# Kernel tuning notes

Hardware: AMD Instinct MI355X
Metric: run time of the kernel (lower is better)

The kernel has to match this reference:

```python
import jax, jax.numpy as jnp
import numpy as np

B, S, DIM, N_CONCEPTS, N_LAYERS = 4, 2048, 1024, 2048, 2


def _phase_linear(x, W, b):
    # x: [b,s,d_in,2]; same real linear applied to real and imag components
    return jnp.einsum('bsdp,od->bsop', x, W) + b[:, None]


def _phase_layernorm(x, gamma, beta, eps=1e-5):
    # per-component LayerNorm over the feature dim with shared affine params
    mu = x.mean(axis=-2, keepdims=True)
    var = x.var(axis=-2, keepdims=True)
    return (x - mu) / jnp.sqrt(var + eps) * gamma[:, None] + beta[:, None]


def setup_inputs() -> dict:
    key = jax.random.key(0)
    ks = jax.random.split(key, 8)
    x = jax.random.normal(ks[0], (B, S, DIM, 2), dtype=jnp.float32)
    concept_memory = jax.random.normal(ks[1], (N_CONCEPTS, DIM, 2), dtype=jnp.float32) * 0.02
    scale = 1.0 / np.sqrt(DIM)
    W_layers = jax.random.normal(ks[2], (N_LAYERS, DIM, DIM), dtype=jnp.float32) * scale
    b_layers = jnp.zeros((N_LAYERS, DIM), dtype=jnp.float32)
    gamma = jnp.ones((N_LAYERS, DIM), dtype=jnp.float32)
    beta = jnp.zeros((N_LAYERS, DIM), dtype=jnp.float32)
    W_out = jax.random.normal(ks[3], (DIM, DIM), dtype=jnp.float32) * scale
    b_out = jnp.zeros((DIM,), dtype=jnp.float32)
    g_out = jnp.ones((DIM,), dtype=jnp.float32)
    beta_out = jnp.zeros((DIM,), dtype=jnp.float32)
    return {"x": x, "concept_memory": concept_memory, "W_layers": W_layers,
            "b_layers": b_layers, "gamma": gamma, "beta": beta,
            "W_out": W_out, "b_out": b_out, "g_out": g_out, "beta_out": beta_out}


def reference(x, concept_memory, W_layers, b_layers, gamma, beta, W_out, b_out, g_out, beta_out):
    xr, xi = x[..., 0], x[..., 1]                       # [b,s,d]
    cr, ci = concept_memory[..., 0], concept_memory[..., 1]  # [n,d]
    # phase-coherence concept attention
    dot_real = jnp.einsum('bsd,nd->bsn', xr, cr) + jnp.einsum('bsd,nd->bsn', xi, ci)
    x_mag = jnp.sqrt((xr ** 2 + xi ** 2).sum(axis=-1, keepdims=True) + 1e-8)   # [b,s,1]
    c_mag = jnp.sqrt((cr ** 2 + ci ** 2).sum(axis=-1) + 1e-8)                  # [n]
    coherence = dot_real / (x_mag * c_mag[None, None, :] + 1e-8)
    concept_attn = jax.nn.softmax(coherence * 2.0, axis=-1)
    concept_retrieved = jnp.einsum('bsn,ndp->bsdp', concept_attn, concept_memory)
    h = x + concept_retrieved * 0.1
    # gated FFN blocks (eval mode: dropout off)
    for l in range(N_LAYERS):
        residual = h
        h = _phase_layernorm(h, gamma[l], beta[l])
        h = _phase_linear(h, W_layers[l], b_layers[l])
        h = jax.nn.gelu(h[..., 0:1], approximate=False) * h
        h = residual + h * 0.1
    out = _phase_layernorm(h, g_out, beta_out)
    out = _phase_linear(out, W_out, b_out)
    return out
```

## Files before the change

### kernel.cpp

```cpp
#include <hip/hip_runtime.h>
#include <hip/hip_bf16.h>

#define ROWS 8192
#define K2   2048
#define NCPT 2048
#define DIMD 1024

using short8 = __attribute__((ext_vector_type(8))) short;
using f32x4  = __attribute__((ext_vector_type(4))) float;

__device__ __forceinline__ unsigned short f2b(float f) {
  __hip_bfloat16 h = __float2bfloat16(f);
  return *reinterpret_cast<unsigned short*>(&h);
}
__device__ __forceinline__ float b2f(unsigned short u) {
  unsigned int x = ((unsigned int)u) << 16;
  return __uint_as_float(x);
}

__device__ __forceinline__ void store_bf16x8(unsigned short* dst, const float4& a, const float4& b) {
  union { unsigned short u[8]; uint4 q; } p;
  p.u[0]=f2b(a.x); p.u[1]=f2b(a.y); p.u[2]=f2b(a.z); p.u[3]=f2b(a.w);
  p.u[4]=f2b(b.x); p.u[5]=f2b(b.y); p.u[6]=f2b(b.z); p.u[7]=f2b(b.w);
  *reinterpret_cast<uint4*>(dst) = p.q;
}
__device__ __forceinline__ void store_bf16x4(unsigned short* dst, float a, float b, float c, float d) {
  union { unsigned short u[4]; uint2 q; } p;
  p.u[0]=f2b(a); p.u[1]=f2b(b); p.u[2]=f2b(c); p.u[3]=f2b(d);
  *reinterpret_cast<uint2*>(dst) = p.q;
}

__device__ __forceinline__ void async_lds16(const void* g, void* l) {
  __builtin_amdgcn_global_load_lds((__attribute__((address_space(1))) void*)g,
                                   (__attribute__((address_space(3))) void*)l, 16, 0, 0);
}

__global__ void cast_row_mag(const float* __restrict__ src, unsigned short* __restrict__ dst,
                             float* __restrict__ mag, int ncol) {
  __shared__ float sred[4];
  int row = blockIdx.x, t = threadIdx.x;
  const float* s = src + (size_t)row * ncol;
  unsigned short* d = dst + (size_t)row * ncol;
  float ss = 0.f;
  for (int i = t * 8; i < ncol; i += 2048) {
    float4 a = *(const float4*)(s + i);
    float4 b = *(const float4*)(s + i + 4);
    ss += a.x*a.x + a.y*a.y + a.z*a.z + a.w*a.w;
    ss += b.x*b.x + b.y*b.y + b.z*b.z + b.w*b.w;
    store_bf16x8(d + i, a, b);
  }
  int lane = t & 63, w = t >> 6;
  for (int o = 32; o; o >>= 1) ss += __shfl_down(ss, o);
  if (lane == 0) sred[w] = ss;
  __syncthreads();
  if (t == 0) mag[row] = sqrtf(sred[0] + sred[1] + sred[2] + sred[3] + 1e-8f);
}

__global__ void cast_f2b(const float* __restrict__ src, unsigned short* __restrict__ dst, int n) {
  int stride = gridDim.x * blockDim.x * 8;
  for (int i = (blockIdx.x * blockDim.x + threadIdx.x) * 8; i < n; i += stride) {
    float4 a = *(const float4*)(src + i);
    float4 b = *(const float4*)(src + i + 4);
    store_bf16x8(dst + i, a, b);
  }
}

__global__ void transpose_f2b(const float* __restrict__ src, unsigned short* __restrict__ dst, int n) {
  __shared__ float tile[32][33];
  int bx = blockIdx.x * 32;
  int by = blockIdx.y * 32;
  int tx = threadIdx.x & 31, ty = threadIdx.x >> 5;
  #pragma unroll
  for (int i = ty; i < 32; i += 8)
    tile[i][tx] = src[(size_t)(by + i) * n + bx + tx];
  __syncthreads();
  #pragma unroll
  for (int i = ty; i < 32; i += 8)
    dst[(size_t)(bx + i) * n + by + tx] = f2b(tile[tx][i]);
}

__global__ void softmax_attn(const unsigned short* __restrict__ logit, unsigned short* __restrict__ attn) {
  __shared__ float sred[4];
  int row = blockIdx.x, t = threadIdx.x;
  int lane = t & 63, w = t >> 6;
  const unsigned short* lr = logit + (size_t)row * NCPT + t * 8;
  short8 lv = *reinterpret_cast<const short8*>(lr);
  float l[8];
  #pragma unroll
  for (int i = 0; i < 8; ++i) l[i] = b2f((unsigned short)lv[i]);
  float m = l[0];
  #pragma unroll
  for (int i = 1; i < 8; ++i) m = fmaxf(m, l[i]);
  for (int o = 32; o; o >>= 1) m = fmaxf(m, __shfl_down(m, o));
  if (lane == 0) sred[w] = m;
  __syncthreads();
  m = fmaxf(fmaxf(sred[0], sred[1]), fmaxf(sred[2], sred[3]));
  __syncthreads();
  float e[8], s = 0.f;
  #pragma unroll
  for (int i = 0; i < 8; ++i) { e[i] = expf(l[i] - m); s += e[i]; }
  for (int o = 32; o; o >>= 1) s += __shfl_down(s, o);
  if (lane == 0) sred[w] = s;
  __syncthreads();
  s = sred[0] + sred[1] + sred[2] + sred[3];
  float inv = 1.f / s;
  float4 A = make_float4(e[0]*inv, e[1]*inv, e[2]*inv, e[3]*inv);
  float4 B = make_float4(e[4]*inv, e[5]*inv, e[6]*inv, e[7]*inv);
  store_bf16x8(attn + (size_t)row * NCPT + t * 8, A, B);
}

__global__ void phase_ln(const unsigned short* __restrict__ h, const float* __restrict__ gamma,
                         const float* __restrict__ beta, unsigned short* __restrict__ out) {
  __shared__ float4 s4[4];
  int bs = blockIdx.x, t = threadIdx.x;
  const unsigned short* hr = h + (size_t)bs * 2048 + t * 8;
  short8 hv = *reinterpret_cast<const short8*>(hr);
  float r0 = b2f((unsigned short)hv[0]), i0 = b2f((unsigned short)hv[1]);
  float r1 = b2f((unsigned short)hv[2]), i1 = b2f((unsigned short)hv[3]);
  float r2 = b2f((unsigned short)hv[4]), i2 = b2f((unsigned short)hv[5]);
  float r3 = b2f((unsigned short)hv[6]), i3 = b2f((unsigned short)hv[7]);
  float4 s;
  s.x = r0 + r1 + r2 + r3;
  s.y = r0*r0 + r1*r1 + r2*r2 + r3*r3;
  s.z = i0 + i1 + i2 + i3;
  s.w = i0*i0 + i1*i1 + i2*i2 + i3*i3;
  int lane = t & 63, w = t >> 6;
  for (int o = 32; o; o >>= 1) {
    s.x += __shfl_down(s.x, o); s.y += __shfl_down(s.y, o);
    s.z += __shfl_down(s.z, o); s.w += __shfl_down(s.w, o);
  }
  if (lane == 0) s4[w] = s;
  __syncthreads();
  float4 T = s4[0];
  #pragma unroll
  for (int i = 1; i < 4; ++i) { T.x += s4[i].x; T.y += s4[i].y; T.z += s4[i].z; T.w += s4[i].w; }
  const float invd = 1.f / 1024.f;
  float mu_r = T.x * invd, var_r = T.y * invd - mu_r * mu_r;
  float mu_i = T.z * invd, var_i = T.w * invd - mu_i * mu_i;
  float is_r = 1.f / sqrtf(var_r + 1e-5f);
  float is_i = 1.f / sqrtf(var_i + 1e-5f);
  float4 g = *(const float4*)(gamma + t * 4);
  float4 b = *(const float4*)(beta + t * 4);
  unsigned short* o0 = out + (size_t)(2 * bs) * 1024 + t * 4;
  unsigned short* o1 = out + (size_t)(2 * bs + 1) * 1024 + t * 4;
  store_bf16x4(o0, (r0-mu_r)*is_r*g.x + b.x, (r1-mu_r)*is_r*g.y + b.y,
                   (r2-mu_r)*is_r*g.z + b.z, (r3-mu_r)*is_r*g.w + b.w);
  store_bf16x4(o1, (i0-mu_i)*is_i*g.x + b.x, (i1-mu_i)*is_i*g.y + b.y,
                   (i2-mu_i)*is_i*g.z + b.z, (i3-mu_i)*is_i*g.w + b.w);
}

template <int EPI>
__global__ __launch_bounds__(512, 2) void gemm256(
    const unsigned short* __restrict__ A, const unsigned short* __restrict__ B,
    int M, int N, int K, void* __restrict__ Cv, const float* __restrict__ aux,
    const float* __restrict__ aux2, const unsigned short* __restrict__ auxb) {
  __shared__ char lds[131072];
  const int t = threadIdx.x;
  const int l = t & 63;
  const int wid = t >> 6;
  const int wm = wid >> 2, wn = wid & 3;

  const int nwg = gridDim.x * gridDim.y;
  int bid = blockIdx.y * gridDim.x + blockIdx.x;
  const int chunk = nwg >> 3;
  bid = (bid & 7) * chunk + (bid >> 3);
  const int row0 = (bid / gridDim.x) * 256;
  const int col0 = (bid % gridDim.x) * 256;

  const int NT = K >> 6;
  const int l15 = l & 15, l7 = l & 7, lk = l >> 4;

  f32x4 acc[8][4] = {};
  short8 af[4][2], bf[4][2];

  auto stage = [&](const unsigned short* gmat, int tileRow, int kcol, char* region) {
    const int rsub = t >> 3;
    const int csw = ((t & 7) ^ (rsub & 7)) << 3;
    const unsigned short* g0 = gmat + (size_t)(tileRow + rsub) * K + kcol + csw;
    async_lds16(g0, region + (t & ~63) * 16);
    async_lds16(g0 + (size_t)64 * K, region + 8192 + (t & ~63) * 16);
  };

  stage(A, row0,       0, lds + 0);
  stage(A, row0 + 128, 0, lds + 16384);
  stage(B, col0,       0, lds + 32768);
  stage(B, col0 + 128, 0, lds + 49152);
  if (NT > 1) {
    stage(A, row0,       64, lds + 65536 + 0);
    stage(A, row0 + 128, 64, lds + 65536 + 16384);
    stage(B, col0,       64, lds + 65536 + 32768);
    stage(B, col0 + 128, 64, lds + 65536 + 49152);
    asm volatile("s_waitcnt vmcnt(8)" ::: "memory");
  } else {
    asm volatile("s_waitcnt vmcnt(0)" ::: "memory");
  }
  __builtin_amdgcn_s_barrier();
  asm volatile("" ::: "memory");

  for (int tk = 0; tk < NT; ++tk) {
    char* bufC = lds + (tk & 1) * 65536;
    const bool pf = (tk + 2 < NT);
    const int kpf = (tk + 2) * 64;

    #pragma unroll
    for (int m = 0; m < 4; ++m)
      #pragma unroll
      for (int kh = 0; kh < 2; ++kh) {
        const int r = wm * 64 + m * 16 + l15;
        const int sp = ((((kh << 2) | lk) ^ l7) << 4);
        af[m][kh] = *reinterpret_cast<const short8*>(bufC + r * 128 + sp);
      }
    #pragma unroll
    for (int n = 0; n < 2; ++n)
      #pragma unroll
      for (int kh = 0; kh < 2; ++kh) {
        const int r = wn * 32 + n * 16 + l15;
        const int sp = ((((kh << 2) | lk) ^ l7) << 4);
        bf[n][kh] = *reinterpret_cast<const short8*>(bufC + 32768 + r * 128 + sp);
      }
    asm volatile("s_waitcnt lgkmcnt(8)" ::: "memory");
    __builtin_amdgcn_s_barrier();
    asm volatile("" ::: "memory");
    __builtin_amdgcn_s_setprio(1);
    #pragma unroll
    for (int kh = 0; kh < 2; ++kh)
      #pragma unroll
      for (int m = 0; m < 4; ++m)
        #pragma unroll
        for (int n = 0; n < 2; ++n)
          acc[m][n] = __builtin_amdgcn_mfma_f32_16x16x32_bf16(af[m][kh], bf[n][kh], acc[m][n], 0, 0, 0);
    __builtin_amdgcn_s_setprio(0);
    asm volatile("" ::: "memory");
    __builtin_amdgcn_s_barrier();
    asm volatile("" ::: "memory");

    #pragma unroll
    for (int n = 2; n < 4; ++n)
      #pragma unroll
      for (int kh = 0; kh < 2; ++kh) {
        const int r = wn * 32 + (n & 1) * 16 + l15;
        const int sp = ((((kh << 2) | lk) ^ l7) << 4);
        bf[n][kh] = *reinterpret_cast<const short8*>(bufC + 49152 + r * 128 + sp);
      }
    if (pf) {
      stage(A, row0,       kpf, bufC + 0);
      stage(B, col0,       kpf, bufC + 32768);
    }
    asm volatile("" ::: "memory");
    __builtin_amdgcn_s_barrier();
    asm volatile("" ::: "memory");
    __builtin_amdgcn_s_setprio(1);
    #pragma unroll
    for (int kh = 0; kh < 2; ++kh)
      #pragma unroll
      for (int m = 0; m < 4; ++m)
        #pragma unroll
        for (int n = 2; n < 4; ++n)
          acc[m][n] = __builtin_amdgcn_mfma_f32_16x16x32_bf16(af[m][kh], bf[n][kh], acc[m][n], 0, 0, 0);
    __builtin_amdgcn_s_setprio(0);
    asm volatile("" ::: "memory");
    __builtin_amdgcn_s_barrier();
    asm volatile("" ::: "memory");

    #pragma unroll
    for (int m = 0; m < 4; ++m)
      #pragma unroll
      for (int kh = 0; kh < 2; ++kh) {
        const int r = wm * 64 + m * 16 + l15;
        const int sp = ((((kh << 2) | lk) ^ l7) << 4);
        af[m][kh] = *reinterpret_cast<const short8*>(bufC + 16384 + r * 128 + sp);
      }
    if (pf) stage(B, col0 + 128, kpf, bufC + 49152);
    asm volatile("" ::: "memory");
    __builtin_amdgcn_s_barrier();
    asm volatile("" ::: "memory");
    __builtin_amdgcn_s_setprio(1);
    #pragma unroll
    for (int kh = 0; kh < 2; ++kh)
      #pragma unroll
      for (int m = 0; m < 4; ++m)
        #pragma unroll
        for (int n = 0; n < 2; ++n)
          acc[m + 4][n] = __builtin_amdgcn_mfma_f32_16x16x32_bf16(af[m][kh], bf[n][kh], acc[m + 4][n], 0, 0, 0);
    __builtin_amdgcn_s_setprio(0);
    asm volatile("" ::: "memory");
    __builtin_amdgcn_s_barrier();
    asm volatile("" ::: "memory");

    if (pf) {
      stage(A, row0 + 128, kpf, bufC + 16384);
      asm volatile("s_waitcnt vmcnt(8)" ::: "memory");
    } else {
      asm volatile("s_waitcnt vmcnt(0)" ::: "memory");
    }
    __builtin_amdgcn_s_barrier();
    asm volatile("" ::: "memory");
    __builtin_amdgcn_s_setprio(1);
    #pragma unroll
    for (int kh = 0; kh < 2; ++kh)
      #pragma unroll
      for (int m = 0; m < 4; ++m)
        #pragma unroll
        for (int n = 2; n < 4; ++n)
          acc[m + 4][n] = __builtin_amdgcn_mfma_f32_16x16x32_bf16(af[m][kh], bf[n][kh], acc[m + 4][n], 0, 0, 0);
    __builtin_amdgcn_s_setprio(0);
    asm volatile("" ::: "memory");
    __builtin_amdgcn_s_barrier();
    asm volatile("" ::: "memory");
  }
  asm volatile("s_waitcnt vmcnt(0)" ::: "memory");

  const int cr = lk * 4;
  #pragma unroll
  for (int m = 0; m < 8; ++m) {
    const int gr = row0 + ((m >> 2) << 7) + wm * 64 + ((m & 3) << 4) + cr;
    #pragma unroll
    for (int n = 0; n < 4; ++n) {
      const int gc = col0 + ((n >> 1) << 7) + wn * 32 + ((n & 1) << 4) + l15;
      if constexpr (EPI == 0) {
        unsigned short* C = (unsigned short*)Cv;
        const float cm_ = aux2[gc];
        #pragma unroll
        for (int j = 0; j < 4; ++j) {
          const int r = gr + j;
          float v = 2.f * acc[m][n][j] / (aux[r] * cm_ + 1e-8f);
          C[(size_t)r * N + gc] = f2b(v);
        }
      } else if constexpr (EPI == 1) {
        unsigned short* C = (unsigned short*)Cv;
        #pragma unroll
        for (int j = 0; j < 4; ++j) {
          const int r = gr + j;
          C[(size_t)r * N + gc] = f2b(b2f(auxb[(size_t)r * N + gc]) + 0.1f * acc[m][n][j]);
        }
      } else if constexpr (EPI == 2) {
        unsigned short* C = (unsigned short*)Cv;
        const float bb = aux[gc];
        #pragma unroll
        for (int jj = 0; jj < 2; ++jj) {
          const int r = gr + jj * 2;
          float re = acc[m][n][jj * 2] + bb;
          float im = acc[m][n][jj * 2 + 1] + bb;
          float g = 0.5f * re * (1.f + erff(re * 0.70710678118654752440f));
          size_t idx = (size_t)(r >> 1) * 2048 + (size_t)gc * 2;
          unsigned int hv = *(unsigned int*)(C + idx);
          float hx = b2f((unsigned short)(hv & 0xffff));
          float hy = b2f((unsigned short)(hv >> 16));
          hx += 0.1f * g * re;
          hy += 0.1f * g * im;
          unsigned int packed = (unsigned int)f2b(hx) | ((unsigned int)f2b(hy) << 16);
          *(unsigned int*)(C + idx) = packed;
        }
      } else {
        float* C = (float*)Cv;
        #pragma unroll
        for (int j = 0; j < 4; ++j) {
          const int r = gr + j;
          C[(size_t)(r >> 1) * 2048 + (size_t)gc * 2 + (r & 1)] = acc[m][n][j] + aux[gc];
        }
      }
    }
  }
}

extern "C" void kernel_launch(void* const* d_in, const int* in_sizes, int n_in,
                              void* d_out, int out_size, void* d_ws, size_t ws_size,
                              hipStream_t stream) {
  const float* x     = (const float*)d_in[0];
  const float* cm    = (const float*)d_in[1];
  const float* Wl    = (const float*)d_in[2];
  const float* bl    = (const float*)d_in[3];
  const float* gamma = (const float*)d_in[4];
  const float* beta  = (const float*)d_in[5];
  const float* Wo    = (const float*)d_in[6];
  const float* bo    = (const float*)d_in[7];
  const float* go    = (const float*)d_in[8];
  const float* bto   = (const float*)d_in[9];
  float* out = (float*)d_out;

  char* p = (char*)d_ws;
  unsigned short* x_bf = (unsigned short*)p; p += (size_t)ROWS * K2 * 2;
  unsigned short* c_bf = (unsigned short*)p; p += (size_t)NCPT * K2 * 2;
  unsigned short* c_T  = (unsigned short*)p; p += (size_t)K2 * NCPT * 2;
  unsigned short* w_bf = (unsigned short*)p; p += (size_t)3 * 1024 * 1024 * 2;
  float* x_mag = (float*)p; p += (size_t)ROWS * 4;
  float* c_mag = (float*)p; p += (size_t)NCPT * 4;
  unsigned short* dot_bf = (unsigned short*)p; p += (size_t)ROWS * NCPT * 2;
  unsigned short* attn   = (unsigned short*)p; p += (size_t)ROWS * NCPT * 2;
  unsigned short* h      = (unsigned short*)p; p += (size_t)ROWS * K2 * 2;
  unsigned short* ln_bf = attn;

  cast_row_mag<<<ROWS, 256, 0, stream>>>(x, x_bf, x_mag, K2);
  cast_row_mag<<<NCPT, 256, 0, stream>>>(cm, c_bf, c_mag, K2);
  transpose_f2b<<<dim3(64, 64), 256, 0, stream>>>(cm, c_T, 2048);
  cast_f2b<<<1024, 256, 0, stream>>>(Wl, w_bf, 2 * 1024 * 1024);
  cast_f2b<<<512, 256, 0, stream>>>(Wo, w_bf + 2 * 1024 * 1024, 1024 * 1024);

  gemm256<0><<<dim3(NCPT / 256, ROWS / 256), 512, 0, stream>>>(
      x_bf, c_bf, ROWS, NCPT, K2, dot_bf, x_mag, c_mag, nullptr);
  softmax_attn<<<ROWS, 256, 0, stream>>>(dot_bf, attn);
  gemm256<1><<<dim3(K2 / 256, ROWS / 256), 512, 0, stream>>>(
      attn, c_T, ROWS, K2, NCPT, h, nullptr, nullptr, x_bf);

  for (int l = 0; l < 2; ++l) {
    phase_ln<<<ROWS, 256, 0, stream>>>(h, gamma + l * 1024, beta + l * 1024, ln_bf);
    gemm256<2><<<dim3(DIMD / 256, 2 * ROWS / 256), 512, 0, stream>>>(
        ln_bf, w_bf + (size_t)l * 1024 * 1024, 2 * ROWS, DIMD, DIMD, h, bl + l * 1024, nullptr, nullptr);
  }

  phase_ln<<<ROWS, 256, 0, stream>>>(h, go, bto, ln_bf);
  gemm256<3><<<dim3(DIMD / 256, 2 * ROWS / 256), 512, 0, stream>>>(
      ln_bf, w_bf + 2 * 1024 * 1024, 2 * ROWS, DIMD, DIMD, out, bo, nullptr, nullptr);
}
```

Measured before the change: 396.5 us.

## Restructure GEMM main loop to prefetch next B fragments and cut barriers

Rewrites the 256x256 bf16 MFMA GEMM inner loop so each k-step runs four MFMA quadrants with separate register sets for the two B halves. The next tile's first B fragments are read from LDS at the end of the current iteration, and one barrier per iteration is removed. The aim is to hide LDS read latency behind MFMA work and cut synchronisation. The explicit lgkmcnt wait is dropped and the vmcnt wait count changes, so correctness relies on compiler-inserted waits and on the new staging order not overwriting buffers that are still being read.

```diff
diff --git a/kernel.cpp b/kernel.cpp
--- a/kernel.cpp
+++ b/kernel.cpp
@@ -171,7 +171,9 @@
   const int l15 = l & 15, l7 = l & 7, lk = l >> 4;
 
   f32x4 acc[8][4] = {};
-  short8 af[4][2], bf[4][2];
+  short8 afA[4][2];
+  short8 bfA[2][2];
+  short8 bfB[2][2];
 
   auto stage = [&](const unsigned short* gmat, int tileRow, int kcol, char* region) {
     const int rsub = t >> 3;
@@ -179,6 +181,17 @@
     const unsigned short* g0 = gmat + (size_t)(tileRow + rsub) * K + kcol + csw;
     async_lds16(g0, region + (t & ~63) * 16);
     async_lds16(g0 + (size_t)64 * K, region + 8192 + (t & ~63) * 16);
+  };
+
+  auto rdA = [&](const char* base, int m, int kh) -> short8 {
+    const int r = wm * 64 + m * 16 + l15;
+    const int sp = ((((kh << 2) | lk) ^ l7) << 4);
+    return *reinterpret_cast<const short8*>(base + r * 128 + sp);
+  };
+  auto rdB = [&](const char* base, int n, int kh) -> short8 {
+    const int r = wn * 32 + n * 16 + l15;
+    const int sp = ((((kh << 2) | lk) ^ l7) << 4);
+    return *reinterpret_cast<const short8*>(base + r * 128 + sp);
   };
 
   stage(A, row0,       0, lds + 0);
@@ -197,30 +210,41 @@
   __builtin_amdgcn_s_barrier();
   asm volatile("" ::: "memory");
 
+  #pragma unroll
+  for (int n = 0; n < 2; ++n)
+    #pragma unroll
+    for (int kh = 0; kh < 2; ++kh)
+      bfA[n][kh] = rdB(lds + 32768, n, kh);
+
   for (int tk = 0; tk < NT; ++tk) {
     char* bufC = lds + (tk & 1) * 65536;
+    char* bufN = lds + (((tk + 1) & 1) * 65536);
     const bool pf = (tk + 2 < NT);
     const int kpf = (tk + 2) * 64;
 
     #pragma unroll
     for (int m = 0; m < 4; ++m)
       #pragma unroll
-      for (int kh = 0; kh < 2; ++kh) {
-        const int r = wm * 64 + m * 16 + l15;
-        const int sp = ((((kh << 2) | lk) ^ l7) << 4);
-        af[m][kh] = *reinterpret_cast<const short8*>(bufC + r * 128 + sp);
-      }
+      for (int kh = 0; kh < 2; ++kh)
+        afA[m][kh] = rdA(bufC + 0, m, kh);
+    __builtin_amdgcn_s_setprio(1);
+    #pragma unroll
+    for (int kh = 0; kh < 2; ++kh)
+      #pragma unroll
+      for (int m = 0; m < 4; ++m)
+        #pragma unroll
+        for (int n = 0; n < 2; ++n)
+          acc[m][n] = __builtin_amdgcn_mfma_f32_16x16x32_bf16(afA[m][kh], bfA[n][kh], acc[m][n], 0, 0, 0);
+    __builtin_amdgcn_s_setprio(0);
     #pragma unroll
     for (int n = 0; n < 2; ++n)
       #pragma unroll
-      for (int kh = 0; kh < 2; ++kh) {
-        const int r = wn * 32 + n * 16 + l15;
-        const int sp = ((((kh << 2) | lk) ^ l7) << 4);
-        bf[n][kh] = *reinterpret_cast<const short8*>(bufC + 32768 + r * 128 + sp);
-      }
-    asm volatile("s_waitcnt lgkmcnt(8)" ::: "memory");
+      for (int kh = 0; kh < 2; ++kh)
+        bfB[n][kh] = rdB(bufC + 49152, n, kh);
+    asm volatile("" ::: "memory");
     __builtin_amdgcn_s_barrier();
     asm volatile("" ::: "memory");
+
     __builtin_amdgcn_s_setprio(1);
     #pragma unroll
     for (int kh = 0; kh < 2; ++kh)
@@ -228,83 +252,57 @@
       for (int m = 0; m < 4; ++m)
         #pragma unroll
         for (int n = 0; n < 2; ++n)
-          acc[m][n] = __builtin_amdgcn_mfma_f32_16x16x32_bf16(af[m][kh], bf[n][kh], acc[m][n], 0, 0, 0);
+          acc[m][n + 2] = __builtin_amdgcn_mfma_f32_16x16x32_bf16(afA[m][kh], bfB[n][kh], acc[m][n + 2], 0, 0, 0);
     __builtin_amdgcn_s_setprio(0);
+    if (pf) {
+      stage(A, row0, kpf, bufC + 0);
+      stage(B, col0, kpf, bufC + 32768);
+    }
     asm volatile("" ::: "memory");
     __builtin_amdgcn_s_barrier();
     asm volatile("" ::: "memory");
 
     #pragma unroll
-    for (int n = 2; n < 4; ++n)
-      #pragma unroll
-      for (int kh = 0; kh < 2; ++kh) {
-        const int r = wn * 32 + (n & 1) * 16 + l15;
-        const int sp = ((((kh << 2) | lk) ^ l7) << 4);
-        bf[n][kh] = *reinterpret_cast<const short8*>(bufC + 49152 + r * 128 + sp);
-      }
+    for (int m = 0; m < 4; ++m)
+      #pragma unroll
+      for (int kh = 0; kh < 2; ++kh)
+        afA[m][kh] = rdA(bufC + 16384, m, kh);
+    __builtin_amdgcn_s_setprio(1);
+    #pragma unroll
+    for (int kh = 0; kh < 2; ++kh)
+      #pragma unroll
+      for (int m = 0; m < 4; ++m)
+        #pragma unroll
+        for (int n = 0; n < 2; ++n)
+          acc[m + 4][n] = __builtin_amdgcn_mfma_f32_16x16x32_bf16(afA[m][kh], bfA[n][kh], acc[m + 4][n], 0, 0, 0);
+    __builtin_amdgcn_s_setprio(0);
+    if (pf) stage(B, col0 + 128, kpf, bufC + 49152);
+    asm volatile("" ::: "memory");
+    __builtin_amdgcn_s_barrier();
+    asm volatile("" ::: "memory");
+
+    __builtin_amdgcn_s_setprio(1);
+    #pragma unroll
+    for (int kh = 0; kh < 2; ++kh)
+      #pragma unroll
+      for (int m = 0; m < 4; ++m)
+        #pragma unroll
+        for (int n = 0; n < 2; ++n)
+          acc[m + 4][n + 2] = __builtin_amdgcn_mfma_f32_16x16x32_bf16(afA[m][kh], bfB[n][kh], acc[m + 4][n + 2], 0, 0, 0);
+    __builtin_amdgcn_s_setprio(0);
+    if (pf) stage(A, row0 + 128, kpf, bufC + 16384);
+    if (tk + 1 < NT) {
+      #pragma unroll
+      for (int n = 0; n < 2; ++n)
+        #pragma unroll
+        for (int kh = 0; kh < 2; ++kh)
+          bfA[n][kh] = rdB(bufN + 32768, n, kh);
+    }
     if (pf) {
-      stage(A, row0,       kpf, bufC + 0);
-      stage(B, col0,       kpf, bufC + 32768);
-    }
-    asm volatile("" ::: "memory");
-    __builtin_amdgcn_s_barrier();
-    asm volatile("" ::: "memory");
-    __builtin_amdgcn_s_setprio(1);
-    #pragma unroll
-    for (int kh = 0; kh < 2; ++kh)
-      #pragma unroll
-      for (int m = 0; m < 4; ++m)
-        #pragma unroll
-        for (int n = 2; n < 4; ++n)
-          acc[m][n] = __builtin_amdgcn_mfma_f32_16x16x32_bf16(af[m][kh], bf[n][kh], acc[m][n], 0, 0, 0);
-    __builtin_amdgcn_s_setprio(0);
-    asm volatile("" ::: "memory");
-    __builtin_amdgcn_s_barrier();
-    asm volatile("" ::: "memory");
-
-    #pragma unroll
-    for (int m = 0; m < 4; ++m)
-      #pragma unroll
-      for (int kh = 0; kh < 2; ++kh) {
-        const int r = wm * 64 + m * 16 + l15;
-        const int sp = ((((kh << 2) | lk) ^ l7) << 4);
-        af[m][kh] = *reinterpret_cast<const short8*>(bufC + 16384 + r * 128 + sp);
-      }
-    if (pf) stage(B, col0 + 128, kpf, bufC + 49152);
-    asm volatile("" ::: "memory");
-    __builtin_amdgcn_s_barrier();
-    asm volatile("" ::: "memory");
-    __builtin_amdgcn_s_setprio(1);
-    #pragma unroll
-    for (int kh = 0; kh < 2; ++kh)
-      #pragma unroll
-      for (int m = 0; m < 4; ++m)
-        #pragma unroll
-        for (int n = 0; n < 2; ++n)
-          acc[m + 4][n] = __builtin_amdgcn_mfma_f32_16x16x32_bf16(af[m][kh], bf[n][kh], acc[m + 4][n], 0, 0, 0);
-    __builtin_amdgcn_s_setprio(0);
-    asm volatile("" ::: "memory");
-    __builtin_amdgcn_s_barrier();
-    asm volatile("" ::: "memory");
-
-    if (pf) {
-      stage(A, row0 + 128, kpf, bufC + 16384);
-      asm volatile("s_waitcnt vmcnt(8)" ::: "memory");
+      asm volatile("s_waitcnt vmcnt(4)" ::: "memory");
     } else {
       asm volatile("s_waitcnt vmcnt(0)" ::: "memory");
     }
-    __builtin_amdgcn_s_barrier();
-    asm volatile("" ::: "memory");
-    __builtin_amdgcn_s_setprio(1);
-    #pragma unroll
-    for (int kh = 0; kh < 2; ++kh)
-      #pragma unroll
-      for (int m = 0; m < 4; ++m)
-        #pragma unroll
-        for (int n = 2; n < 4; ++n)
-          acc[m + 4][n] = __builtin_amdgcn_mfma_f32_16x16x32_bf16(af[m][kh], bf[n][kh], acc[m + 4][n], 0, 0, 0);
-    __builtin_amdgcn_s_setprio(0);
-    asm volatile("" ::: "memory");
     __builtin_amdgcn_s_barrier();
     asm volatile("" ::: "memory");
   }
```

Result: faster. 363.6 us (-8.3%).
